# Kernel tuning notes

Hardware: AMD Instinct MI355X
Metric: run time of the kernel (lower is better)

## Reference

```python
import jax, jax.numpy as jnp
import numpy as np

NB_HEAD = 16
SIZE_PER_HEAD = 64
D_MODEL = 1024
OUT_DIM = NB_HEAD * SIZE_PER_HEAD
BIG_NEG = 1e10


def setup_inputs() -> dict:
    key = jax.random.key(0)
    ks = jax.random.split(key, 6)
    B, L = 2, 2048
    q = jax.random.normal(ks[0], (B, L, D_MODEL), dtype=jnp.float32)
    k = jax.random.normal(ks[1], (B, L, D_MODEL), dtype=jnp.float32)
    v = jax.random.normal(ks[2], (B, L, D_MODEL), dtype=jnp.float32)
    v_mask = jnp.ones((B, L), dtype=jnp.float32)
    q_mask = jnp.ones((B, L), dtype=jnp.float32)
    # glorot_normal-ish init for the three projection kernels
    std = (2.0 / (D_MODEL + OUT_DIM)) ** 0.5
    q_kernel = jax.random.normal(ks[3], (D_MODEL, OUT_DIM), dtype=jnp.float32) * std
    k_kernel = jax.random.normal(ks[4], (D_MODEL, OUT_DIM), dtype=jnp.float32) * std
    v_kernel = jax.random.normal(ks[5], (D_MODEL, OUT_DIM), dtype=jnp.float32) * std
    return {"q": q, "k": k, "v": v, "v_mask": v_mask, "q_mask": q_mask,
            "q_kernel": q_kernel, "k_kernel": k_kernel, "v_kernel": v_kernel}


def reference(q, k, v, v_mask, q_mask, q_kernel, k_kernel, v_kernel):
    B, Lq, _ = q.shape
    Lk = k.shape[1]
    H, D = NB_HEAD, SIZE_PER_HEAD
    # projections -> [B, L, H, D]
    qw = (q @ q_kernel).reshape(B, Lq, H, D)
    kw = (k @ k_kernel).reshape(B, Lk, H, D)
    vw = (v @ v_kernel).reshape(B, Lk, H, D)
    # scaled dot-product scores [B, H, Lq, Lk]
    scores = jnp.einsum('bqhd,bkhd->bhqk', qw, kw) / jnp.sqrt(jnp.float32(D))
    # additive key mask (original permutes so mask broadcasts over key axis)
    scores = scores - (1.0 - v_mask)[:, None, None, :] * BIG_NEG
    a = jax.nn.softmax(scores, axis=-1)
    # weighted sum -> [B, Lq, H, D] -> [B, Lq, H*D]
    o = jnp.einsum('bhqk,bkhd->bqhd', a, vw).reshape(B, Lq, H * D)
    # multiplicative query mask on output
    o = o * q_mask[:, :, None]
    return o
```

## Files before the change

### kernel.cpp

```cpp
#include <hip/hip_runtime.h>
#include <hip/hip_bf16.h>

#define B_SZ 2
#define SEQ  2048
#define DM   1024
#define NH   16
#define HD   64

typedef __attribute__((ext_vector_type(8))) short bf16x8;
typedef __attribute__((ext_vector_type(4))) short bf16x4;
typedef __attribute__((ext_vector_type(4))) float f32x4;
typedef __attribute__((ext_vector_type(16))) float f32x16;

__device__ __forceinline__ short f2b(float f) {
    __hip_bfloat16 h = __float2bfloat16(f);
    return *reinterpret_cast<short*>(&h);
}

__device__ __forceinline__ int cvtpk(float a, float b) {
    int r;
    asm("v_cvt_pk_bf16_f32 %0, %1, %2" : "=v"(r) : "v"(a), "v"(b));
    return r;
}

__device__ __forceinline__ void async_copy16(void* lds, const void* g) {
    __builtin_amdgcn_global_load_lds(
        (const __attribute__((address_space(1))) void*)g,
        (__attribute__((address_space(3))) void*)lds, 16, 0, 0);
}

__global__ __launch_bounds__(256) void kPre(
    const float* __restrict__ q, const float* __restrict__ k, const float* __restrict__ v,
    const float* __restrict__ w0, const float* __restrict__ w1, const float* __restrict__ w2,
    short* __restrict__ qb, short* __restrict__ kb, short* __restrict__ vb,
    short* __restrict__ t0, short* __restrict__ t1, short* __restrict__ t2) {
    int z = blockIdx.z, tid = threadIdx.x;
    if (z < 3) {
        const float* src = z == 0 ? q : (z == 1 ? k : v);
        short*       dst = z == 0 ? qb : (z == 1 ? kb : vb);
        size_t i = ((size_t)blockIdx.x * 256 + tid) * 8;
        float4 a0 = *reinterpret_cast<const float4*>(src + i);
        float4 a1 = *reinterpret_cast<const float4*>(src + i + 4);
        bf16x8 c;
        c[0] = f2b(a0.x); c[1] = f2b(a0.y); c[2] = f2b(a0.z); c[3] = f2b(a0.w);
        c[4] = f2b(a1.x); c[5] = f2b(a1.y); c[6] = f2b(a1.z); c[7] = f2b(a1.w);
        *reinterpret_cast<bf16x8*>(dst + i) = c;
    } else {
        if (blockIdx.x >= 256) return;
        const float* w = z == 3 ? w0 : (z == 4 ? w1 : w2);
        short*       t = z == 3 ? t0 : (z == 4 ? t1 : t2);
        __shared__ float tile[64][65];
        int n0 = (blockIdx.x & 15) * 64, k0 = (blockIdx.x >> 4) * 64;
        int c = tid & 63, rr = tid >> 6;
#pragma unroll
        for (int i = 0; i < 16; i++) {
            int kk = i * 4 + rr;
            tile[kk][c] = w[(size_t)(k0 + kk) * DM + n0 + c];
        }
        __syncthreads();
#pragma unroll
        for (int i = 0; i < 16; i++) {
            int nn = i * 4 + rr;
            t[(size_t)(n0 + nn) * DM + k0 + c] = f2b(tile[c][nn]);
        }
    }
}

__global__ __launch_bounds__(256) void kProj(
    const short* __restrict__ qb, const short* __restrict__ kb, const short* __restrict__ vb,
    const short* __restrict__ wtq, const short* __restrict__ wtk, const short* __restrict__ wtv,
    short* __restrict__ qw, short* __restrict__ kw, short* __restrict__ vwT) {
    int z = blockIdx.z;
    const short* A  = z == 0 ? qb : (z == 1 ? kb : vb);
    const short* Bt = z == 0 ? wtq : (z == 1 ? wtk : wtv);

    __shared__ short As[128 * 64];
    __shared__ short Bs[128 * 64];

    int tid = threadIdx.x;
    int m0 = blockIdx.y * 128, n0 = blockIdx.x * 128;
    int wv = tid >> 6, lane = tid & 63, quad = lane >> 4, ln = lane & 15;
    int rblk = (wv >> 1) * 64, cblk = (wv & 1) * 64;

    int rA = wv * 32;
    int srow = rA + (lane >> 3), scol = (lane & 7) * 8;

    f32x4 zero = {0.f, 0.f, 0.f, 0.f};
    f32x4 acc[4][4];
#pragma unroll
    for (int rt = 0; rt < 4; rt++)
#pragma unroll
        for (int ct = 0; ct < 4; ct++) acc[rt][ct] = zero;

    for (int ks = 0; ks < DM; ks += 64) {
        const short* gA = A  + (size_t)(m0 + srow) * DM + ks + scol;
        const short* gB = Bt + (size_t)(n0 + srow) * DM + ks + scol;
#pragma unroll
        for (int i = 0; i < 4; i++) {
            async_copy16(&As[(rA + i * 8) * 64], gA + (size_t)i * 8 * DM);
            async_copy16(&Bs[(rA + i * 8) * 64], gB + (size_t)i * 8 * DM);
        }
        __syncthreads();
#pragma unroll
        for (int kc = 0; kc < 2; kc++) {
            bf16x8 af[4], bfv[4];
#pragma unroll
            for (int rt = 0; rt < 4; rt++)
                af[rt] = *reinterpret_cast<bf16x8*>(&As[(rblk + rt * 16 + ln) * 64 + kc * 32 + quad * 8]);
#pragma unroll
            for (int ct = 0; ct < 4; ct++)
                bfv[ct] = *reinterpret_cast<bf16x8*>(&Bs[(cblk + ct * 16 + ln) * 64 + kc * 32 + quad * 8]);
#pragma unroll
            for (int rt = 0; rt < 4; rt++)
#pragma unroll
                for (int ct = 0; ct < 4; ct++)
                    acc[rt][ct] = __builtin_amdgcn_mfma_f32_16x16x32_bf16(
                        af[rt], bfv[ct], acc[rt][ct], 0, 0, 0);
        }
        __syncthreads();
    }

    if (z < 2) {
        short* C = z == 0 ? qw : kw;
#pragma unroll
        for (int rt = 0; rt < 4; rt++)
#pragma unroll
            for (int r = 0; r < 4; r++) {
                int row = m0 + rblk + rt * 16 + quad * 4 + r;
#pragma unroll
                for (int ct = 0; ct < 4; ct++)
                    C[(size_t)row * DM + n0 + cblk + ct * 16 + ln] = f2b(acc[rt][ct][r]);
            }
    } else {
#pragma unroll
        for (int rt = 0; rt < 4; rt++) {
            int srow0 = m0 + rblk + rt * 16 + quad * 4;
            int bb = srow0 >> 11, lk = srow0 & (SEQ - 1);
#pragma unroll
            for (int ct = 0; ct < 4; ct++) {
                int coln = n0 + cblk + ct * 16 + ln;
                int hh = coln >> 6, dd = coln & 63;
                bf16x4 pk;
                pk[0] = f2b(acc[rt][ct][0]); pk[1] = f2b(acc[rt][ct][1]);
                pk[2] = f2b(acc[rt][ct][2]); pk[3] = f2b(acc[rt][ct][3]);
                *reinterpret_cast<bf16x4*>(
                    &vwT[(((size_t)bb * NH + hh) * HD + dd) * SEQ + lk]) = pk;
            }
        }
    }
}

__global__ __launch_bounds__(256, 3) void kAttn(
    const short* __restrict__ qw, const short* __restrict__ kw, const short* __restrict__ vwT,
    const float* __restrict__ vmask, const float* __restrict__ qmask, float* __restrict__ out) {
    int b = blockIdx.z, h = blockIdx.y, lq0 = blockIdx.x * 128;
    int tid = threadIdx.x, wv = tid >> 6, lane = tid & 63;
    int l5 = lane & 31, half = lane >> 5;

    __shared__ short Ks[128][72];
    __shared__ short Vt[64][136];

    const short* qrow = qw + (size_t)(b * SEQ + lq0 + wv * 32 + l5) * DM + h * HD;
    bf16x8 qf[4];
#pragma unroll
    for (int ki = 0; ki < 4; ki++)
        qf[ki] = *reinterpret_cast<const bf16x8*>(qrow + ki * 16 + half * 8);

    float lrow = 0.f;
    f32x16 o0, o1;
#pragma unroll
    for (int i = 0; i < 16; i++) { o0[i] = 0.f; o1[i] = 0.f; }

    int krow = tid >> 1, kcol = (tid & 1) * 32;
    int vrow = tid >> 2, vcol = (tid & 3) * 32;
    const short* kp = kw + (size_t)(b * SEQ + krow) * DM + h * HD + kcol;
    const short* vp = vwT + ((size_t)(b * NH + h) * HD + vrow) * SEQ + vcol;
    const float* vmb = vmask + b * SEQ;

    const float C1 = 0.18033688011f;
    const float C2 = 1.4426950e10f;

    bf16x8 kr[4], vr[4];
#pragma unroll
    for (int i = 0; i < 4; i++) {
        kr[i] = *reinterpret_cast<const bf16x8*>(kp + i * 8);
        vr[i] = *reinterpret_cast<const bf16x8*>(vp + i * 8);
    }

    for (int it = 0; it < SEQ / 128; it++) {
        int lk0 = it * 128;
#pragma unroll
        for (int i = 0; i < 4; i++) {
            *reinterpret_cast<bf16x8*>(&Ks[krow][kcol + i * 8]) = kr[i];
            *reinterpret_cast<bf16x8*>(&Vt[vrow][vcol + i * 8]) = vr[i];
        }
        __syncthreads();

        if (it + 1 < SEQ / 128) {
            kp += (size_t)128 * DM;
            vp += 128;
#pragma unroll
            for (int i = 0; i < 4; i++) {
                kr[i] = *reinterpret_cast<const bf16x8*>(kp + i * 8);
                vr[i] = *reinterpret_cast<const bf16x8*>(vp + i * 8);
            }
        }

        float rs = 0.f;
#pragma unroll
        for (int lt = 0; lt < 4; lt++) {
            f32x16 s;
#pragma unroll
            for (int i = 0; i < 16; i++) s[i] = 0.f;
#pragma unroll
            for (int ki = 0; ki < 4; ki++) {
                bf16x8 kf = *reinterpret_cast<bf16x8*>(&Ks[lt * 32 + l5][ki * 16 + half * 8]);
                s = __builtin_amdgcn_mfma_f32_32x32x16_bf16(kf, qf[ki], s, 0, 0, 0);
            }

            float p[16];
#pragma unroll
            for (int g = 0; g < 4; g++) {
                float4 mv = *reinterpret_cast<const float4*>(
                    &vmb[lk0 + lt * 32 + 8 * g + 4 * half]);
                float p0 = __builtin_amdgcn_exp2f(fmaf(s[4 * g + 0], C1, fmaf(mv.x, C2, -C2)));
                float p1 = __builtin_amdgcn_exp2f(fmaf(s[4 * g + 1], C1, fmaf(mv.y, C2, -C2)));
                float p2 = __builtin_amdgcn_exp2f(fmaf(s[4 * g + 2], C1, fmaf(mv.z, C2, -C2)));
                float p3 = __builtin_amdgcn_exp2f(fmaf(s[4 * g + 3], C1, fmaf(mv.w, C2, -C2)));
                rs += (p0 + p1) + (p2 + p3);
                p[4 * g + 0] = p0; p[4 * g + 1] = p1;
                p[4 * g + 2] = p2; p[4 * g + 3] = p3;
            }

            int wA = cvtpk(p[0],  p[1]),  wB = cvtpk(p[2],  p[3]);
            int wC = cvtpk(p[4],  p[5]),  wD = cvtpk(p[6],  p[7]);
            int wE = cvtpk(p[8],  p[9]),  wF = cvtpk(p[10], p[11]);
            int wG = cvtpk(p[12], p[13]), wH = cvtpk(p[14], p[15]);
            int xA = __shfl_xor(wA, 32), xB = __shfl_xor(wB, 32);
            int xC = __shfl_xor(wC, 32), xD = __shfl_xor(wD, 32);
            int xE = __shfl_xor(wE, 32), xF = __shfl_xor(wF, 32);
            int xG = __shfl_xor(wG, 32), xH = __shfl_xor(wH, 32);
            bool lo = (half == 0);
            union { int i[4]; bf16x8 v; } uA, uB;
            uA.i[0] = lo ? wA : xC; uA.i[1] = lo ? wB : xD;
            uA.i[2] = lo ? xA : wC; uA.i[3] = lo ? xB : wD;
            uB.i[0] = lo ? wE : xG; uB.i[1] = lo ? wF : xH;
            uB.i[2] = lo ? xE : wG; uB.i[3] = lo ? xF : wH;

            bf16x8 vf00 = *reinterpret_cast<bf16x8*>(&Vt[l5]     [(2 * lt) * 16 + half * 8]);
            bf16x8 vf01 = *reinterpret_cast<bf16x8*>(&Vt[32 + l5][(2 * lt) * 16 + half * 8]);
            bf16x8 vf10 = *reinterpret_cast<bf16x8*>(&Vt[l5]     [(2 * lt + 1) * 16 + half * 8]);
            bf16x8 vf11 = *reinterpret_cast<bf16x8*>(&Vt[32 + l5][(2 * lt + 1) * 16 + half * 8]);
            o0 = __builtin_amdgcn_mfma_f32_32x32x16_bf16(vf00, uA.v, o0, 0, 0, 0);
            o1 = __builtin_amdgcn_mfma_f32_32x32x16_bf16(vf01, uA.v, o1, 0, 0, 0);
            o0 = __builtin_amdgcn_mfma_f32_32x32x16_bf16(vf10, uB.v, o0, 0, 0, 0);
            o1 = __builtin_amdgcn_mfma_f32_32x32x16_bf16(vf11, uB.v, o1, 0, 0, 0);
        }

        rs += __shfl_xor(rs, 32);
        lrow += rs;
        __syncthreads();
    }

    int lq = lq0 + wv * 32 + l5;
    float sc2 = (1.0f / lrow) * qmask[b * SEQ + lq];
    float* orow = out + (size_t)(b * SEQ + lq) * DM + h * HD;
#pragma unroll
    for (int g = 0; g < 4; g++) {
        float4 st0, st1;
        st0.x = o0[4 * g + 0] * sc2; st0.y = o0[4 * g + 1] * sc2;
        st0.z = o0[4 * g + 2] * sc2; st0.w = o0[4 * g + 3] * sc2;
        st1.x = o1[4 * g + 0] * sc2; st1.y = o1[4 * g + 1] * sc2;
        st1.z = o1[4 * g + 2] * sc2; st1.w = o1[4 * g + 3] * sc2;
        *reinterpret_cast<float4*>(&orow[8 * g + 4 * half]) = st0;
        *reinterpret_cast<float4*>(&orow[32 + 8 * g + 4 * half]) = st1;
    }
}

extern "C" void kernel_launch(void* const* d_in, const int* in_sizes, int n_in,
                              void* d_out, int out_size, void* d_ws, size_t ws_size,
                              hipStream_t stream) {
    const float* q  = (const float*)d_in[0];
    const float* k  = (const float*)d_in[1];
    const float* v  = (const float*)d_in[2];
    const float* vm = (const float*)d_in[3];
    const float* qm = (const float*)d_in[4];
    const float* qk = (const float*)d_in[5];
    const float* kk = (const float*)d_in[6];
    const float* vk = (const float*)d_in[7];
    float* out = (float*)d_out;

    short* ws  = (short*)d_ws;
    short* wtq = ws;
    short* wtk = wtq + 1024 * 1024;
    short* wtv = wtk + 1024 * 1024;
    short* vb  = wtv + 1024 * 1024;
    short* qw  = vb + (size_t)4096 * 1024;
    short* kw  = qw + (size_t)4096 * 1024;
    short* vwT = kw + (size_t)4096 * 1024;
    short* qb = (short*)d_out;
    short* kb = qb + (size_t)4096 * 1024;

    kPre <<<dim3(2048, 1, 6), 256, 0, stream>>>(q, k, v, qk, kk, vk,
                                                qb, kb, vb, wtq, wtk, wtv);
    kProj<<<dim3(8, 32, 3), 256, 0, stream>>>(qb, kb, vb, wtq, wtk, wtv, qw, kw, vwT);
    kAttn<<<dim3(16, 16, 2), 256, 0, stream>>>(qw, kw, vwT, vm, qm, out);
}
```

Baseline: 238.4 us.

## Split key tiles across wave pairs in attention, halving query rows per block

Each attention block now covers 64 query rows instead of 128. Its four waves form two pairs, and each pair handles half of every 128-key tile. The partial outputs and row sums are combined through shared memory at the end. This doubles the grid to 1024 blocks and raises the occupancy hint, aiming to fill more CUs on a device with many compute units. In exchange, every K/V tile is loaded from global memory twice as often overall, and the kernel adds an end-of-kernel reduction and barrier.

```diff
diff --git a/kernel.cpp b/kernel.cpp
--- a/kernel.cpp
+++ b/kernel.cpp
@@ -150,17 +150,18 @@
     }
 }
 
-__global__ __launch_bounds__(256, 3) void kAttn(
+__global__ __launch_bounds__(256, 4) void kAttn(
     const short* __restrict__ qw, const short* __restrict__ kw, const short* __restrict__ vwT,
     const float* __restrict__ vmask, const float* __restrict__ qmask, float* __restrict__ out) {
-    int b = blockIdx.z, h = blockIdx.y, lq0 = blockIdx.x * 128;
+    int b = blockIdx.z, h = blockIdx.y, lq0 = blockIdx.x * 64;
     int tid = threadIdx.x, wv = tid >> 6, lane = tid & 63;
     int l5 = lane & 31, half = lane >> 5;
+    int g = wv & 1, h2 = wv >> 1;
 
     __shared__ short Ks[128][72];
     __shared__ short Vt[64][136];
 
-    const short* qrow = qw + (size_t)(b * SEQ + lq0 + wv * 32 + l5) * DM + h * HD;
+    const short* qrow = qw + (size_t)(b * SEQ + lq0 + g * 32 + l5) * DM + h * HD;
     bf16x8 qf[4];
 #pragma unroll
     for (int ki = 0; ki < 4; ki++)
@@ -208,28 +209,29 @@
 
         float rs = 0.f;
 #pragma unroll
-        for (int lt = 0; lt < 4; lt++) {
+        for (int lt = 0; lt < 2; lt++) {
+            int LT = h2 * 2 + lt;
             f32x16 s;
 #pragma unroll
             for (int i = 0; i < 16; i++) s[i] = 0.f;
 #pragma unroll
             for (int ki = 0; ki < 4; ki++) {
-                bf16x8 kf = *reinterpret_cast<bf16x8*>(&Ks[lt * 32 + l5][ki * 16 + half * 8]);
+                bf16x8 kf = *reinterpret_cast<bf16x8*>(&Ks[LT * 32 + l5][ki * 16 + half * 8]);
                 s = __builtin_amdgcn_mfma_f32_32x32x16_bf16(kf, qf[ki], s, 0, 0, 0);
             }
 
             float p[16];
 #pragma unroll
-            for (int g = 0; g < 4; g++) {
+            for (int g4 = 0; g4 < 4; g4++) {
                 float4 mv = *reinterpret_cast<const float4*>(
-                    &vmb[lk0 + lt * 32 + 8 * g + 4 * half]);
-                float p0 = __builtin_amdgcn_exp2f(fmaf(s[4 * g + 0], C1, fmaf(mv.x, C2, -C2)));
-                float p1 = __builtin_amdgcn_exp2f(fmaf(s[4 * g + 1], C1, fmaf(mv.y, C2, -C2)));
-                float p2 = __builtin_amdgcn_exp2f(fmaf(s[4 * g + 2], C1, fmaf(mv.z, C2, -C2)));
-                float p3 = __builtin_amdgcn_exp2f(fmaf(s[4 * g + 3], C1, fmaf(mv.w, C2, -C2)));
+                    &vmb[lk0 + LT * 32 + 8 * g4 + 4 * half]);
+                float p0 = __builtin_amdgcn_exp2f(fmaf(s[4 * g4 + 0], C1, fmaf(mv.x, C2, -C2)));
+                float p1 = __builtin_amdgcn_exp2f(fmaf(s[4 * g4 + 1], C1, fmaf(mv.y, C2, -C2)));
+                float p2 = __builtin_amdgcn_exp2f(fmaf(s[4 * g4 + 2], C1, fmaf(mv.z, C2, -C2)));
+                float p3 = __builtin_amdgcn_exp2f(fmaf(s[4 * g4 + 3], C1, fmaf(mv.w, C2, -C2)));
                 rs += (p0 + p1) + (p2 + p3);
-                p[4 * g + 0] = p0; p[4 * g + 1] = p1;
-                p[4 * g + 2] = p2; p[4 * g + 3] = p3;
+                p[4 * g4 + 0] = p0; p[4 * g4 + 1] = p1;
+                p[4 * g4 + 2] = p2; p[4 * g4 + 3] = p3;
             }
 
             int wA = cvtpk(p[0],  p[1]),  wB = cvtpk(p[2],  p[3]);
@@ -247,10 +249,10 @@
             uB.i[0] = lo ? wE : xG; uB.i[1] = lo ? wF : xH;
             uB.i[2] = lo ? xE : wG; uB.i[3] = lo ? xF : wH;
 
-            bf16x8 vf00 = *reinterpret_cast<bf16x8*>(&Vt[l5]     [(2 * lt) * 16 + half * 8]);
-            bf16x8 vf01 = *reinterpret_cast<bf16x8*>(&Vt[32 + l5][(2 * lt) * 16 + half * 8]);
-            bf16x8 vf10 = *reinterpret_cast<bf16x8*>(&Vt[l5]     [(2 * lt + 1) * 16 + half * 8]);
-            bf16x8 vf11 = *reinterpret_cast<bf16x8*>(&Vt[32 + l5][(2 * lt + 1) * 16 + half * 8]);
+            bf16x8 vf00 = *reinterpret_cast<bf16x8*>(&Vt[l5]     [(2 * LT) * 16 + half * 8]);
+            bf16x8 vf01 = *reinterpret_cast<bf16x8*>(&Vt[32 + l5][(2 * LT) * 16 + half * 8]);
+            bf16x8 vf10 = *reinterpret_cast<bf16x8*>(&Vt[l5]     [(2 * LT + 1) * 16 + half * 8]);
+            bf16x8 vf11 = *reinterpret_cast<bf16x8*>(&Vt[32 + l5][(2 * LT + 1) * 16 + half * 8]);
             o0 = __builtin_amdgcn_mfma_f32_32x32x16_bf16(vf00, uA.v, o0, 0, 0, 0);
             o1 = __builtin_amdgcn_mfma_f32_32x32x16_bf16(vf01, uA.v, o1, 0, 0, 0);
             o0 = __builtin_amdgcn_mfma_f32_32x32x16_bf16(vf10, uB.v, o0, 0, 0, 0);
@@ -262,18 +264,36 @@
         __syncthreads();
     }
 
-    int lq = lq0 + wv * 32 + l5;
+    float* cb = reinterpret_cast<float*>(&Ks[0][0]);
+    float* lr = reinterpret_cast<float*>(&Vt[0][0]);
+    int ci = g * 64 + lane;
+    if (h2 == 1) {
+#pragma unroll
+        for (int i = 0; i < 16; i++) cb[ci + 128 * i]        = o0[i];
+#pragma unroll
+        for (int i = 0; i < 16; i++) cb[ci + 128 * (16 + i)] = o1[i];
+        lr[ci] = lrow;
+    }
+    __syncthreads();
+    if (h2 == 1) return;
+#pragma unroll
+    for (int i = 0; i < 16; i++) o0[i] += cb[ci + 128 * i];
+#pragma unroll
+    for (int i = 0; i < 16; i++) o1[i] += cb[ci + 128 * (16 + i)];
+    lrow += lr[ci];
+
+    int lq = lq0 + g * 32 + l5;
     float sc2 = (1.0f / lrow) * qmask[b * SEQ + lq];
     float* orow = out + (size_t)(b * SEQ + lq) * DM + h * HD;
 #pragma unroll
-    for (int g = 0; g < 4; g++) {
+    for (int g4 = 0; g4 < 4; g4++) {
         float4 st0, st1;
-        st0.x = o0[4 * g + 0] * sc2; st0.y = o0[4 * g + 1] * sc2;
-        st0.z = o0[4 * g + 2] * sc2; st0.w = o0[4 * g + 3] * sc2;
-        st1.x = o1[4 * g + 0] * sc2; st1.y = o1[4 * g + 1] * sc2;
-        st1.z = o1[4 * g + 2] * sc2; st1.w = o1[4 * g + 3] * sc2;
-        *reinterpret_cast<float4*>(&orow[8 * g + 4 * half]) = st0;
-        *reinterpret_cast<float4*>(&orow[32 + 8 * g + 4 * half]) = st1;
+        st0.x = o0[4 * g4 + 0] * sc2; st0.y = o0[4 * g4 + 1] * sc2;
+        st0.z = o0[4 * g4 + 2] * sc2; st0.w = o0[4 * g4 + 3] * sc2;
+        st1.x = o1[4 * g4 + 0] * sc2; st1.y = o1[4 * g4 + 1] * sc2;
+        st1.z = o1[4 * g4 + 2] * sc2; st1.w = o1[4 * g4 + 3] * sc2;
+        *reinterpret_cast<float4*>(&orow[8 * g4 + 4 * half]) = st0;
+        *reinterpret_cast<float4*>(&orow[32 + 8 * g4 + 4 * half]) = st1;
     }
 }
 
@@ -304,5 +324,5 @@
     kPre <<<dim3(2048, 1, 6), 256, 0, stream>>>(q, k, v, qk, kk, vk,
                                                 qb, kb, vb, wtq, wtk, wtv);
     kProj<<<dim3(8, 32, 3), 256, 0, stream>>>(qb, kb, vb, wtq, wtk, wtv, qw, kw, vwT);
-    kAttn<<<dim3(16, 16, 2), 256, 0, stream>>>(qw, kw, vwT, vm, qm, out);
-}
+    kAttn<<<dim3(32, 16, 2), 256, 0, stream>>>(qw, kw, vwT, vm, qm, out);
+}
```

Result: faster. 230.4 us, median of 2 (-3.3%).
